# Kernel tuning notes

Hardware: AMD Instinct MI355X
Metric: run time of the kernel (lower is better)

Reference implementation:

```python
import jax, jax.numpy as jnp
import numpy as np

CLASSES = 21
IOU_THRESH = 0.5
ALPHA = 0.25   # focal loss alpha
GAMMA = 2.0    # focal loss gamma
SL1_BETA = 1.0 # torch SmoothL1Loss default beta
CLS_W = 1.0
REG_W = 1.0
NUM_ANCHORS = 98304
NUM_TARGETS = 1024


def _compute_iou(boxes_a, boxes_b):
    # boxes_a: [T,4], boxes_b: [A,4] in (x1,y1,x2,y2) -> [T,A]
    lt = jnp.maximum(boxes_a[:, None, :2], boxes_b[None, :, :2])
    rb = jnp.minimum(boxes_a[:, None, 2:], boxes_b[None, :, 2:])
    wh = jnp.clip(rb - lt, 0.0)
    inter = wh[..., 0] * wh[..., 1]
    area_a = (boxes_a[:, 2] - boxes_a[:, 0]) * (boxes_a[:, 3] - boxes_a[:, 1])
    area_b = (boxes_b[:, 2] - boxes_b[:, 0]) * (boxes_b[:, 3] - boxes_b[:, 1])
    union = area_a[:, None] + area_b[None, :] - inter
    return inter / jnp.maximum(union, 1e-8)


def _encode(boxes, anchors):
    bw = boxes[:, 2] - boxes[:, 0]
    bh = boxes[:, 3] - boxes[:, 1]
    bcx = boxes[:, 0] + 0.5 * bw
    bcy = boxes[:, 1] + 0.5 * bh
    aw = anchors[:, 2] - anchors[:, 0]
    ah = anchors[:, 3] - anchors[:, 1]
    acx = anchors[:, 0] + 0.5 * aw
    acy = anchors[:, 1] + 0.5 * ah
    tx = (bcx - acx) / aw
    ty = (bcy - acy) / ah
    tw = jnp.log(jnp.maximum(bw, 1e-8) / aw)
    th = jnp.log(jnp.maximum(bh, 1e-8) / ah)
    return jnp.stack([tx, ty, tw, th], axis=1)


def _focal_loss(logits, targets):
    # elementwise sigmoid focal loss (no reduction)
    p = jax.nn.sigmoid(logits)
    # numerically stable BCE with logits
    ce = jnp.maximum(logits, 0.0) - logits * targets + jnp.log1p(jnp.exp(-jnp.abs(logits)))
    p_t = p * targets + (1.0 - p) * (1.0 - targets)
    alpha_t = ALPHA * targets + (1.0 - ALPHA) * (1.0 - targets)
    return alpha_t * (1.0 - p_t) ** GAMMA * ce


def _smooth_l1(diff):
    ad = jnp.abs(diff)
    return jnp.where(ad < SL1_BETA, 0.5 * diff * diff / SL1_BETA, ad - 0.5 * SL1_BETA)


def setup_inputs() -> dict:
    key = jax.random.key(0)
    kA, kW, kT, kJ, kL, kC, kB = jax.random.split(key, 7)
    A, T = NUM_ANCHORS, NUM_TARGETS
    centers = jax.random.uniform(kA, (A, 2), minval=0.15, maxval=0.85)
    sizes = jax.random.uniform(kW, (A, 2), minval=0.05, maxval=0.30)
    anchors = jnp.concatenate([centers - 0.5 * sizes, centers + 0.5 * sizes], axis=1)
    # targets = jittered anchors so IoU >= 0.5 matches exist
    idx = jax.random.randint(kT, (T,), 0, A)
    jitter = jax.random.uniform(kJ, (T, 4), minval=-0.01, maxval=0.01)
    target_boxes = anchors[idx] + jitter
    target_labels = jax.random.randint(kL, (T,), 0, CLASSES)
    classification_preds = jax.random.normal(kC, (A, CLASSES), dtype=jnp.float32)
    boxes_preds = jax.random.normal(kB, (A, 4), dtype=jnp.float32)
    return {
        'classification_preds': classification_preds,
        'boxes_preds': boxes_preds,
        'anchors': anchors,
        'target_boxes': target_boxes,
        'target_labels': target_labels,
    }


def reference(classification_preds, boxes_preds, anchors, target_boxes, target_labels):
    iou = _compute_iou(target_boxes, anchors)  # [T, A]

    # anchor-side matching -> classification targets
    max_iou_for_anchors = jnp.max(iou, axis=0)          # [A]
    target_ids_for_anchors = jnp.argmax(iou, axis=0)     # [A]
    positive_mask = max_iou_for_anchors >= IOU_THRESH    # [A] bool
    n_pos = jnp.sum(positive_mask.astype(jnp.float32))
    onehot = jax.nn.one_hot(target_labels[target_ids_for_anchors], CLASSES, dtype=jnp.float32)
    cls_targets = jnp.where(positive_mask[:, None], onehot, 0.0)
    cls_loss = jnp.sum(_focal_loss(classification_preds, cls_targets)) / n_pos

    max_iou_for_targets = jnp.max(iou, axis=1)          # [T]
    anchor_ids_for_targets = jnp.argmax(iou, axis=1)     # [T]
    t_mask = (max_iou_for_targets >= IOU_THRESH).astype(jnp.float32)  # [T]
    matched_anchors = anchors[anchor_ids_for_targets]    # [T,4]
    encoded = _encode(target_boxes, matched_anchors)     # [T,4]
    pred = boxes_preds[anchor_ids_for_targets]           # [T,4]
    diff = (pred - encoded) * t_mask[:, None]
    n_match = jnp.maximum(jnp.sum(t_mask), 1.0)
    reg_loss = jnp.sum(_smooth_l1(diff)) / (n_match * 4.0)  # mean over matched elements

    w_cls = cls_loss * CLS_W
    w_reg = reg_loss * REG_W
    return (w_cls + w_reg, w_cls, w_reg)
```

## Files before the change

kernel.cpp:

```cpp
#include <hip/hip_runtime.h>
#include <stdint.h>

#define NA 98304
#define NT 1024
#define NC 21
#define ACH 192
#define TCH 8
#define HI_MIN 0xBF000000u


__device__ __forceinline__ float f0(float x) {
    const float ax = fabsf(x);
    const float u  = __expf(-ax);
    const float ce = fmaxf(x, 0.f) + __logf(1.f + u);
    const float p  = (x >= 0.f ? 1.f : u) / (1.f + u);
    return 0.75f * p * p * ce;
}
__device__ __forceinline__ float f1(float x) {
    const float ax = fabsf(x);
    const float u  = __expf(-ax);
    const float ce = fmaxf(x, 0.f) - x + __logf(1.f + u);
    const float p  = (x >= 0.f ? 1.f : u) / (1.f + u);
    const float q  = 1.f - p;
    return 0.25f * q * q * ce;
}

__device__ __forceinline__ unsigned long long mk_key(float iou, unsigned int idx) {
    return ((unsigned long long)(__float_as_uint(iou) | 0x80000000u) << 32) |
           (unsigned long long)(0xFFFFFFFFu - idx);
}

__global__ __launch_bounds__(256) void k_match(
    const float4* __restrict__ anchors,
    const float4* __restrict__ tboxes,
    unsigned long long* __restrict__ akeys,
    unsigned long long* __restrict__ tkeys)
{
    __shared__ float4 s_t[128];
    __shared__ unsigned long long s_tk[128];

    const int tid   = threadIdx.x;
    const int tbase = blockIdx.y * 128;
    const int a0    = blockIdx.x * 512 + tid;
    const int a1    = a0 + 256;

    if (tid < 128) {
        s_t[tid]  = tboxes[tbase + tid];
        s_tk[tid] = 0ull;
    }
    const float4 A0 = anchors[a0];
    const float4 A1 = anchors[a1];
    __syncthreads();

    const float ar0 = (A0.z - A0.x) * (A0.w - A0.y);
    const float ar1 = (A1.z - A1.x) * (A1.w - A1.y);

    float b0 = 0.f, b1 = 0.f;
    int   i0 = -1,  i1 = -1;

    #pragma unroll 4
    for (int t = 0; t < 128; ++t) {
        const float4 tb = s_t[t];
        const float sa = (tb.z - tb.x) * (tb.w - tb.y);

        {
            const float lx = fmaxf(A0.x, tb.x);
            const float ly = fmaxf(A0.y, tb.y);
            const float rx = fminf(A0.z, tb.z);
            const float ry = fminf(A0.w, tb.w);
            const float w  = fmaxf(rx - lx, 0.f);
            const float h  = fmaxf(ry - ly, 0.f);
            const float inter = w * h;
            const float uni = (ar0 + sa) - inter;
            if (__builtin_expect(inter + inter >= uni, 0)) {
                const float iou = inter / uni;
                if (iou > b0) { b0 = iou; i0 = t; }
                atomicMax(&s_tk[t], mk_key(iou, (unsigned int)a0));
            }
        }
        {
            const float lx = fmaxf(A1.x, tb.x);
            const float ly = fmaxf(A1.y, tb.y);
            const float rx = fminf(A1.z, tb.z);
            const float ry = fminf(A1.w, tb.w);
            const float w  = fmaxf(rx - lx, 0.f);
            const float h  = fmaxf(ry - ly, 0.f);
            const float inter = w * h;
            const float uni = (ar1 + sa) - inter;
            if (__builtin_expect(inter + inter >= uni, 0)) {
                const float iou = inter / uni;
                if (iou > b1) { b1 = iou; i1 = t; }
                atomicMax(&s_tk[t], mk_key(iou, (unsigned int)a1));
            }
        }
    }

    if (i0 >= 0) atomicMax(&akeys[a0], mk_key(b0, (unsigned int)(tbase + i0)));
    if (i1 >= 0) atomicMax(&akeys[a1], mk_key(b1, (unsigned int)(tbase + i1)));

    __syncthreads();
    if (tid < 128) {
        const unsigned long long tk = s_tk[tid];
        if (tk != 0ull) atomicMax(&tkeys[tbase + tid], tk);
    }
}

__global__ __launch_bounds__(256) void k_cls(
    const float4* __restrict__ preds4,
    const float* __restrict__ preds,
    const int* __restrict__ tlabels,
    const unsigned long long* __restrict__ akeys,
    double* __restrict__ loss_part,
    int* __restrict__ n_part)
{
    __shared__ float s_red[4];
    __shared__ int   s_cnt[2];

    const int tid = threadIdx.x;
    const int blk = blockIdx.x;

    float acc = 0.f;

    bool valid = false;
    if (tid < 128) {
        const unsigned long long k = akeys[blk * 128 + tid];
        if ((unsigned int)(k >> 32) >= HI_MIN) {
            valid = true;
            const int lab = tlabels[0xFFFFFFFFu - (unsigned int)k];
            const float x = preds[(blk * 128 + tid) * NC + lab];
            acc += f1(x) - f0(x);
        }
    }
    const unsigned long long bal = __ballot(valid);

    const int pbase = blk * 672;
    #pragma unroll
    for (int j = 0; j < 3; ++j) {
        const int i = tid + j * 256;
        if (i < 672) {
            const float4 v = preds4[pbase + i];
            acc += (f0(v.x) + f0(v.y)) + (f0(v.z) + f0(v.w));
        }
    }

    for (int o = 32; o > 0; o >>= 1) acc += __shfl_down(acc, o);
    const int lane = tid & 63, wid = tid >> 6;
    if (lane == 0) {
        s_red[wid] = acc;
        if (wid < 2) s_cnt[wid] = (int)__popcll(bal);
    }
    __syncthreads();
    if (tid == 0) {
        atomicAdd(&loss_part[blk & 63],
                  (double)(s_red[0] + s_red[1] + s_red[2] + s_red[3]));
        atomicAdd(&n_part[blk & 15], s_cnt[0] + s_cnt[1]);
    }
}

__device__ __forceinline__ float smooth_l1(float d) {
    const float ad = fabsf(d);
    return (ad < 1.f) ? 0.5f * d * d : ad - 0.5f;
}

__global__ __launch_bounds__(1024) void k_final(
    const float4* __restrict__ anchors,
    const float4* __restrict__ tboxes,
    const float4* __restrict__ bpreds,
    const unsigned long long* __restrict__ tkeys,
    const double* __restrict__ loss_part,
    const int* __restrict__ n_part,
    float* __restrict__ out)
{
    const int tid = threadIdx.x;

    float s = 0.f, m = 0.f;
    {
        const unsigned long long key = tkeys[tid];
        if ((unsigned int)(key >> 32) >= HI_MIN) {
            const unsigned int ga = 0xFFFFFFFFu - (unsigned int)key;
            const float4 tb  = tboxes[tid];
            const float4 abx = anchors[ga];
            const float4 pb  = bpreds[ga];
            const float bw = tb.z - tb.x, bh = tb.w - tb.y;
            const float bcx = tb.x + 0.5f * bw, bcy = tb.y + 0.5f * bh;
            const float aw = abx.z - abx.x, ah = abx.w - abx.y;
            const float acx = abx.x + 0.5f * aw, acy = abx.y + 0.5f * ah;
            const float tx = (bcx - acx) / aw;
            const float ty = (bcy - acy) / ah;
            const float tw = logf(fmaxf(bw, 1e-8f) / aw);
            const float th = logf(fmaxf(bh, 1e-8f) / ah);
            s = smooth_l1(pb.x - tx) + smooth_l1(pb.y - ty) +
                smooth_l1(pb.z - tw) + smooth_l1(pb.w - th);
            m = 1.f;
        }
    }
    for (int o = 32; o > 0; o >>= 1) {
        s += __shfl_down(s, o);
        m += __shfl_down(m, o);
    }
    __shared__ float s_s[16], s_m[16];
    const int lane = tid & 63, wid = tid >> 6;
    if (lane == 0) { s_s[wid] = s; s_m[wid] = m; }
    __syncthreads();
    if (tid == 0) {
        float rs = 0.f, rm = 0.f;
        for (int i = 0; i < 16; ++i) { rs += s_s[i]; rm += s_m[i]; }
        double cl = 0.0;
        for (int i = 0; i < 64; ++i) cl += loss_part[i];
        int np = 0;
        for (int i = 0; i < 16; ++i) np += n_part[i];
        const float cls = (float)(cl / (double)np);
        const float reg = rs / (fmaxf(rm, 1.f) * 4.f);
        out[0] = cls + reg;
        out[1] = cls;
        out[2] = reg;
    }
}

extern "C" void kernel_launch(void* const* d_in, const int* in_sizes, int n_in,
                              void* d_out, int out_size, void* d_ws, size_t ws_size,
                              hipStream_t stream) {
    const float*  cls_preds = (const float*)d_in[0];
    const float4* bpreds    = (const float4*)d_in[1];
    const float4* anchors   = (const float4*)d_in[2];
    const float4* tboxes    = (const float4*)d_in[3];
    const int*    tlabels   = (const int*)d_in[4];

    char* ws = (char*)d_ws;
    int*    n_part    = (int*)(ws + 0);
    double* loss_part = (double*)(ws + 64);
    unsigned long long* tkeys = (unsigned long long*)(ws + 1024);
    unsigned long long* akeys = (unsigned long long*)(ws + 16384);

    hipMemsetAsync(d_ws, 0, 576, stream);

    k_match<<<dim3(ACH, TCH), 256, 0, stream>>>(anchors, tboxes, akeys, tkeys);
    k_cls<<<NA / 128, 256, 0, stream>>>((const float4*)cls_preds, cls_preds,
                                        tlabels, akeys, loss_part, n_part);
    k_final<<<1, 1024, 0, stream>>>(anchors, tboxes, bpreds, tkeys,
                                    loss_part, n_part, (float*)d_out);
}
```

Measured before the change: 140.8 us.

## Fuse dense focal sum into match kernel and merge cls/final via last-block epilogue

The dense f0 focal-loss pass over all classification logits moves into the IoU matching kernel, which writes per-block partials. The classification correction and the final reduction merge into one 256-block kernel that finishes with a last-block-done counter. The workspace clear moves from a hipMemsetAsync into block 0 of the match kernel, removing a memset and a launch. This cuts launches and overlaps the streaming logit reads with matching compute. It depends on the in-kernel header clear racing correctly with later use, since the accumulators are zeroed in the first kernel and only read by the next.

After: 138.2 us. About the same (-1.8%).

```diff
diff --git a/kernel.cpp b/kernel.cpp
--- a/kernel.cpp
+++ b/kernel.cpp
@@ -6,6 +6,8 @@
 #define NC 21
 #define ACH 192
 #define TCH 8
+#define NBLK (ACH * TCH)
+#define EPB  256
 #define HI_MIN 0xBF000000u
 
 
@@ -24,32 +26,53 @@
     const float q  = 1.f - p;
     return 0.25f * q * q * ce;
 }
-
 __device__ __forceinline__ unsigned long long mk_key(float iou, unsigned int idx) {
     return ((unsigned long long)(__float_as_uint(iou) | 0x80000000u) << 32) |
            (unsigned long long)(0xFFFFFFFFu - idx);
 }
+__device__ __forceinline__ float smooth_l1(float d) {
+    const float ad = fabsf(d);
+    return (ad < 1.f) ? 0.5f * d * d : ad - 0.5f;
+}
 
 __global__ __launch_bounds__(256) void k_match(
     const float4* __restrict__ anchors,
     const float4* __restrict__ tboxes,
+    const float4* __restrict__ preds4,
     unsigned long long* __restrict__ akeys,
-    unsigned long long* __restrict__ tkeys)
+    unsigned long long* __restrict__ tkeys,
+    float* __restrict__ f0_part,
+    unsigned* __restrict__ hdr)
 {
     __shared__ float4 s_t[128];
     __shared__ unsigned long long s_tk[128];
+    __shared__ float s_f[4];
 
     const int tid   = threadIdx.x;
+    const int L     = blockIdx.y * ACH + blockIdx.x;
     const int tbase = blockIdx.y * 128;
     const int a0    = blockIdx.x * 512 + tid;
     const int a1    = a0 + 256;
 
+    if (L == 0 && tid < 160) hdr[tid] = 0u;
+
     if (tid < 128) {
         s_t[tid]  = tboxes[tbase + tid];
         s_tk[tid] = 0ull;
     }
     const float4 A0 = anchors[a0];
     const float4 A1 = anchors[a1];
+
+    float facc;
+    {
+        const int pb = L * 336;
+        const float4 v0 = preds4[pb + tid];
+        facc = (f0(v0.x) + f0(v0.y)) + (f0(v0.z) + f0(v0.w));
+        if (tid < 80) {
+            const float4 v1 = preds4[pb + 256 + tid];
+            facc += (f0(v1.x) + f0(v1.y)) + (f0(v1.z) + f0(v1.w));
+        }
+    }
     __syncthreads();
 
     const float ar0 = (A0.z - A0.x) * (A0.w - A0.y);
@@ -62,7 +85,6 @@
     for (int t = 0; t < 128; ++t) {
         const float4 tb = s_t[t];
         const float sa = (tb.z - tb.x) * (tb.w - tb.y);
-
         {
             const float lx = fmaxf(A0.x, tb.x);
             const float ly = fmaxf(A0.y, tb.y);
@@ -98,87 +120,89 @@
     if (i0 >= 0) atomicMax(&akeys[a0], mk_key(b0, (unsigned int)(tbase + i0)));
     if (i1 >= 0) atomicMax(&akeys[a1], mk_key(b1, (unsigned int)(tbase + i1)));
 
+    for (int o = 32; o > 0; o >>= 1) facc += __shfl_down(facc, o);
+    const int lane = tid & 63, wid = tid >> 6;
+    if (lane == 0) s_f[wid] = facc;
+
     __syncthreads();
     if (tid < 128) {
         const unsigned long long tk = s_tk[tid];
         if (tk != 0ull) atomicMax(&tkeys[tbase + tid], tk);
     }
-}
-
-__global__ __launch_bounds__(256) void k_cls(
-    const float4* __restrict__ preds4,
+    if (tid == 0) f0_part[L] = s_f[0] + s_f[1] + s_f[2] + s_f[3];
+}
+
+__global__ __launch_bounds__(256) void k_epi(
     const float* __restrict__ preds,
     const int* __restrict__ tlabels,
+    const float4* __restrict__ anchors,
+    const float4* __restrict__ tboxes,
+    const float4* __restrict__ bpreds,
     const unsigned long long* __restrict__ akeys,
+    const unsigned long long* __restrict__ tkeys,
+    const float* __restrict__ f0_part,
     double* __restrict__ loss_part,
-    int* __restrict__ n_part)
+    int* __restrict__ n_part,
+    int* __restrict__ done,
+    float* __restrict__ out)
 {
     __shared__ float s_red[4];
-    __shared__ int   s_cnt[2];
+    __shared__ int   s_cnt[4];
+    __shared__ int   s_flag;
+    __shared__ float s_s[4], s_m[4];
+    __shared__ double s_dbl[64];
+    __shared__ int    s_int[16];
 
     const int tid = threadIdx.x;
     const int blk = blockIdx.x;
+    const int lane = tid & 63, wid = tid >> 6;
 
     float acc = 0.f;
-
-    bool valid = false;
+    int   cnt = 0;
+    {
+        const int a = blk * 384 + tid;
+        const unsigned long long k = akeys[a];
+        if ((unsigned int)(k >> 32) >= HI_MIN) {
+            cnt = 1;
+            const int lab = tlabels[0xFFFFFFFFu - (unsigned int)k];
+            acc += f1(preds[a * NC + lab]) - f0(preds[a * NC + lab]);
+        }
+    }
     if (tid < 128) {
-        const unsigned long long k = akeys[blk * 128 + tid];
+        const int a = blk * 384 + 256 + tid;
+        const unsigned long long k = akeys[a];
         if ((unsigned int)(k >> 32) >= HI_MIN) {
-            valid = true;
+            cnt += 1;
             const int lab = tlabels[0xFFFFFFFFu - (unsigned int)k];
-            const float x = preds[(blk * 128 + tid) * NC + lab];
-            acc += f1(x) - f0(x);
-        }
-    }
-    const unsigned long long bal = __ballot(valid);
-
-    const int pbase = blk * 672;
-    #pragma unroll
-    for (int j = 0; j < 3; ++j) {
-        const int i = tid + j * 256;
-        if (i < 672) {
-            const float4 v = preds4[pbase + i];
-            acc += (f0(v.x) + f0(v.y)) + (f0(v.z) + f0(v.w));
-        }
-    }
-
-    for (int o = 32; o > 0; o >>= 1) acc += __shfl_down(acc, o);
-    const int lane = tid & 63, wid = tid >> 6;
-    if (lane == 0) {
-        s_red[wid] = acc;
-        if (wid < 2) s_cnt[wid] = (int)__popcll(bal);
-    }
+            acc += f1(preds[a * NC + lab]) - f0(preds[a * NC + lab]);
+        }
+    }
+    if (tid < 6) acc += f0_part[blk * 6 + tid];
+
+    for (int o = 32; o > 0; o >>= 1) {
+        acc += __shfl_down(acc, o);
+        cnt += __shfl_down(cnt, o);
+    }
+    if (lane == 0) { s_red[wid] = acc; s_cnt[wid] = cnt; }
     __syncthreads();
     if (tid == 0) {
         atomicAdd(&loss_part[blk & 63],
                   (double)(s_red[0] + s_red[1] + s_red[2] + s_red[3]));
-        atomicAdd(&n_part[blk & 15], s_cnt[0] + s_cnt[1]);
-    }
-}
-
-__device__ __forceinline__ float smooth_l1(float d) {
-    const float ad = fabsf(d);
-    return (ad < 1.f) ? 0.5f * d * d : ad - 0.5f;
-}
-
-__global__ __launch_bounds__(1024) void k_final(
-    const float4* __restrict__ anchors,
-    const float4* __restrict__ tboxes,
-    const float4* __restrict__ bpreds,
-    const unsigned long long* __restrict__ tkeys,
-    const double* __restrict__ loss_part,
-    const int* __restrict__ n_part,
-    float* __restrict__ out)
-{
-    const int tid = threadIdx.x;
+        atomicAdd(&n_part[blk & 15], s_cnt[0] + s_cnt[1] + s_cnt[2] + s_cnt[3]);
+        __threadfence();
+        s_flag = (atomicAdd(done, 1) == EPB - 1);
+    }
+    __syncthreads();
+    if (!s_flag) return;
 
     float s = 0.f, m = 0.f;
-    {
-        const unsigned long long key = tkeys[tid];
+    #pragma unroll
+    for (int j = 0; j < 4; ++j) {
+        const int t = tid + 256 * j;
+        const unsigned long long key = tkeys[t];
         if ((unsigned int)(key >> 32) >= HI_MIN) {
             const unsigned int ga = 0xFFFFFFFFu - (unsigned int)key;
-            const float4 tb  = tboxes[tid];
+            const float4 tb  = tboxes[t];
             const float4 abx = anchors[ga];
             const float4 pb  = bpreds[ga];
             const float bw = tb.z - tb.x, bh = tb.w - tb.y;
@@ -189,26 +213,28 @@
             const float ty = (bcy - acy) / ah;
             const float tw = logf(fmaxf(bw, 1e-8f) / aw);
             const float th = logf(fmaxf(bh, 1e-8f) / ah);
-            s = smooth_l1(pb.x - tx) + smooth_l1(pb.y - ty) +
-                smooth_l1(pb.z - tw) + smooth_l1(pb.w - th);
-            m = 1.f;
+            s += smooth_l1(pb.x - tx) + smooth_l1(pb.y - ty) +
+                 smooth_l1(pb.z - tw) + smooth_l1(pb.w - th);
+            m += 1.f;
         }
     }
     for (int o = 32; o > 0; o >>= 1) {
         s += __shfl_down(s, o);
         m += __shfl_down(m, o);
     }
-    __shared__ float s_s[16], s_m[16];
-    const int lane = tid & 63, wid = tid >> 6;
+    __syncthreads();
     if (lane == 0) { s_s[wid] = s; s_m[wid] = m; }
+
+    if (tid < 64) s_dbl[tid] = atomicAdd(&loss_part[tid], 0.0);
+    if (tid >= 64 && tid < 80) s_int[tid - 64] = atomicAdd(&n_part[tid - 64], 0);
     __syncthreads();
     if (tid == 0) {
-        float rs = 0.f, rm = 0.f;
-        for (int i = 0; i < 16; ++i) { rs += s_s[i]; rm += s_m[i]; }
         double cl = 0.0;
-        for (int i = 0; i < 64; ++i) cl += loss_part[i];
+        for (int i = 0; i < 64; ++i) cl += s_dbl[i];
         int np = 0;
-        for (int i = 0; i < 16; ++i) np += n_part[i];
+        for (int i = 0; i < 16; ++i) np += s_int[i];
+        const float rs = s_s[0] + s_s[1] + s_s[2] + s_s[3];
+        const float rm = s_m[0] + s_m[1] + s_m[2] + s_m[3];
         const float cls = (float)(cl / (double)np);
         const float reg = rs / (fmaxf(rm, 1.f) * 4.f);
         out[0] = cls + reg;
@@ -220,23 +246,25 @@
 extern "C" void kernel_launch(void* const* d_in, const int* in_sizes, int n_in,
                               void* d_out, int out_size, void* d_ws, size_t ws_size,
                               hipStream_t stream) {
-    const float*  cls_preds = (const float*)d_in[0];
-    const float4* bpreds    = (const float4*)d_in[1];
-    const float4* anchors   = (const float4*)d_in[2];
-    const float4* tboxes    = (const float4*)d_in[3];
-    const int*    tlabels   = (const int*)d_in[4];
+    const float*  preds   = (const float*)d_in[0];
+    const float4* preds4  = (const float4*)d_in[0];
+    const float4* bpreds  = (const float4*)d_in[1];
+    const float4* anchors = (const float4*)d_in[2];
+    const float4* tboxes  = (const float4*)d_in[3];
+    const int*    tlabels = (const int*)d_in[4];
 
     char* ws = (char*)d_ws;
-    int*    n_part    = (int*)(ws + 0);
+    int*    done      = (int*)(ws + 0);
     double* loss_part = (double*)(ws + 64);
-    unsigned long long* tkeys = (unsigned long long*)(ws + 1024);
+    int*    n_part    = (int*)(ws + 576);
+    float*  f0_part   = (float*)(ws + 1024);
+    unsigned long long* tkeys = (unsigned long long*)(ws + 8192);
     unsigned long long* akeys = (unsigned long long*)(ws + 16384);
 
-    hipMemsetAsync(d_ws, 0, 576, stream);
-
-    k_match<<<dim3(ACH, TCH), 256, 0, stream>>>(anchors, tboxes, akeys, tkeys);
-    k_cls<<<NA / 128, 256, 0, stream>>>((const float4*)cls_preds, cls_preds,
-                                        tlabels, akeys, loss_part, n_part);
-    k_final<<<1, 1024, 0, stream>>>(anchors, tboxes, bpreds, tkeys,
-                                    loss_part, n_part, (float*)d_out);
-}
+    k_match<<<dim3(ACH, TCH), 256, 0, stream>>>(anchors, tboxes, preds4,
+                                                akeys, tkeys, f0_part,
+                                                (unsigned*)d_ws);
+    k_epi<<<EPB, 256, 0, stream>>>(preds, tlabels, anchors, tboxes, bpreds,
+                                   akeys, tkeys, f0_part, loss_part, n_part,
+                                   done, (float*)d_out);
+}
```
